# Performance work log

Measured on AMD Instinct MI355X. Metric: run time of the kernel, lower is better.

Reference implementation:

```python
import jax, jax.numpy as jnp
import numpy as np

EPS_BN = 1e-5
EPS_RENORM = 1e-9

def conv_bn_relu(x, W, g, b, m, v):
    # x: [B, Cin, N], W: [Cout, Cin] (1x1 conv, no bias). Eval-mode BN.
    y = jnp.einsum('oi,bin->bon', W, x)
    scale = (g / jnp.sqrt(v + EPS_BN))[None, :, None]
    bias = (b - m * g / jnp.sqrt(v + EPS_BN))[None, :, None]
    return jax.nn.relu(y * scale + bias)

def _make_params(key, cout, cin):
    k1, k2, k3, k4 = jax.random.split(key, 4)
    W = jax.random.normal(k1, (cout, cin), jnp.float32) * (1.0 / np.sqrt(cin))
    g = jax.random.uniform(k2, (cout,), jnp.float32, 0.5, 1.5)
    b = jax.random.normal(k3, (cout,), jnp.float32) * 0.1
    m = jax.random.normal(k4, (cout,), jnp.float32) * 0.1
    v = jax.random.uniform(jax.random.fold_in(key, 7), (cout,), jnp.float32, 0.5, 1.5)
    return W, g, b, m, v

def setup_inputs() -> dict:
    key = jax.random.key(0)
    ks = jax.random.split(key, 6)
    B, C, N = 8, 1024, 2048
    x = jax.random.normal(ks[0], (B, C, N), jnp.float32)
    inp = {'x': x}
    dims = [(1024, 1024), (1024, 1024), (128, 1024), (128, 1024), (1024, 1024)]
    for i, (co, ci) in enumerate(dims):
        W, g, b, m, v = _make_params(ks[i + 1], co, ci)
        inp[f'W{i+1}'] = W
        inp[f'g{i+1}'] = g
        inp[f'b{i+1}'] = b
        inp[f'm{i+1}'] = m
        inp[f'v{i+1}'] = v
    return inp

def reference(x,
              W1, g1, b1, m1, v1,
              W2, g2, b2, m2, v2,
              W3, g3, b3, m3, v3,
              W4, g4, b4, m4, v4,
              W5, g5, b5, m5, v5):
    x1 = conv_bn_relu(x, W1, g1, b1, m1, v1)          # [B,1024,N]
    v_ = conv_bn_relu(x1, W2, g2, b2, m2, v2)         # [B,1024,N]
    q_ = conv_bn_relu(x1, W3, g3, b3, m3, v3)         # [B,128,N]
    k_ = conv_bn_relu(x1, W4, g4, b4, m4, v4)         # [B,128,N]
    # q transposed: [B,N,128] @ [B,128,N] -> [B,N,N]
    scores = jnp.einsum('bcn,bcm->bnm', q_, k_)
    scores = jax.nn.softmax(scores, axis=-1)
    scores = scores / (EPS_RENORM + scores.sum(axis=1, keepdims=True))
    attn = jnp.einsum('bcn,bnm->bcm', v_, scores)     # [B,1024,N]
    x2 = conv_bn_relu(x1 - attn, W5, g5, b5, m5, v5)
    return x1 + x2
```

## Files before the change

kernel.cpp:

```cpp
#include <hip/hip_runtime.h>

typedef unsigned short u16;
using bf16x8 = __attribute__((ext_vector_type(8))) short;
using f32x4  = __attribute__((ext_vector_type(4))) float;

#define CH   1024
#define NP   2048
#define CQ   128

__device__ __forceinline__ float bf2f(u16 u){
  union { unsigned u; float f; } c; c.u = ((unsigned)u) << 16; return c.f;
}
__device__ __forceinline__ u16 f2bf(float f){
  unsigned x = __float_as_uint(f);
  unsigned r = (x + 0x7fffu + ((x >> 16) & 1u)) >> 16;
  return (u16)r;
}

__device__ __forceinline__ void gl2lds16(const u16* g, u16* l){
  __builtin_amdgcn_global_load_lds(
      (const __attribute__((address_space(1))) unsigned int*)(const void*)g,
      (__attribute__((address_space(3))) unsigned int*)(void*)l,
      16, 0, 0);
}

__global__ void ws_marker(float* out, float have_mb){
  out[0] = 1048576.0f + have_mb;
}

__global__ __launch_bounds__(256) void transpose_split(const float* __restrict__ x,
                                                       u16* __restrict__ xh,
                                                       u16* __restrict__ xl){
  const int bb = blockIdx.z;
  const int n0 = blockIdx.x * 64, c0 = blockIdx.y * 64;
  __shared__ float tile[64][65];
  const int t = threadIdx.x;
  const float* xb = x + ((size_t)bb*CH + c0)*NP + n0;
#pragma unroll
  for (int rr = 0; rr < 4; ++rr){
    const int c_l = (t >> 4) + rr*16;
    const int n_l = (t & 15) * 4;
    float4 v = *(const float4*)&xb[(size_t)c_l*NP + n_l];
    tile[c_l][n_l+0] = v.x; tile[c_l][n_l+1] = v.y;
    tile[c_l][n_l+2] = v.z; tile[c_l][n_l+3] = v.w;
  }
  __syncthreads();
  u16* oh = xh + ((size_t)bb*NP + n0)*CH + c0;
  u16* ol = xl + ((size_t)bb*NP + n0)*CH + c0;
#pragma unroll
  for (int rr = 0; rr < 4; ++rr){
    const int n_l = (t >> 4) + rr*16;
    const int c_l = (t & 15) * 4;
    ushort4 h, l;
    float v0 = tile[c_l+0][n_l], v1 = tile[c_l+1][n_l];
    float v2 = tile[c_l+2][n_l], v3 = tile[c_l+3][n_l];
    h.x = f2bf(v0); l.x = f2bf(v0 - bf2f(h.x));
    h.y = f2bf(v1); l.y = f2bf(v1 - bf2f(h.y));
    h.z = f2bf(v2); l.z = f2bf(v2 - bf2f(h.z));
    h.w = f2bf(v3); l.w = f2bf(v3 - bf2f(h.w));
    *(ushort4*)&oh[(size_t)n_l*CH + c_l] = h;
    *(ushort4*)&ol[(size_t)n_l*CH + c_l] = l;
  }
}

__global__ __launch_bounds__(256) void prep_all(
    const float* __restrict__ w0, const float* __restrict__ w1,
    const float* __restrict__ w2, const float* __restrict__ w3,
    const float* __restrict__ w4,
    u16* w1h, u16* w1l, u16* w2h,
    u16* w34h, u16* w34l, u16* w5h,
    const float* g3, const float* b3, const float* m3, const float* v3,
    const float* g4, const float* b4, const float* m4, const float* v4,
    float* p34, float* colsum){
  const int seg = blockIdx.y;
  if (seg == 5){
    for (int i = blockIdx.x*blockDim.x + threadIdx.x; i < 1024; i += gridDim.x*blockDim.x){
      const int grp = i >> 8, j = i & 255;
      const float* pa = (grp==0) ? g3 : (grp==1) ? b3 : (grp==2) ? m3 : v3;
      const float* pb = (grp==0) ? g4 : (grp==1) ? b4 : (grp==2) ? m4 : v4;
      p34[i] = (j < 128) ? pa[j] : pb[j-128];
    }
    return;
  }
  if (seg == 6){
    for (int i = blockIdx.x*blockDim.x + threadIdx.x; i < 8*NP; i += gridDim.x*blockDim.x)
      colsum[i] = 0.f;
    return;
  }
  const float* w; u16 *wh, *wl; int n;
  switch (seg){
    case 0:  w = w0; wh = w1h;           wl = w1l;           n = CH*CH; break;
    case 1:  w = w1; wh = w2h;           wl = nullptr;       n = CH*CH; break;
    case 2:  w = w2; wh = w34h;          wl = w34l;          n = CQ*CH; break;
    case 3:  w = w3; wh = w34h + CQ*CH;  wl = w34l + CQ*CH;  n = CQ*CH; break;
    default: w = w4; wh = w5h;           wl = nullptr;       n = CH*CH; break;
  }
  for (int i = blockIdx.x*blockDim.x + threadIdx.x; i < n; i += gridDim.x*blockDim.x){
    float v = w[i];
    u16 h = f2bf(v);
    wh[i] = h;
    if (wl) wl[i] = f2bf(v - bf2f(h));
  }
}

template<int EPI>
__global__ __launch_bounds__(256, 4) void gemm_plain(
    const u16* __restrict__ A, const u16* __restrict__ B,
    int lda, int ldb, long astr, long bstr, int K,
    void* __restrict__ out0, long ostr, int ldo,
    const float* __restrict__ pg, const float* __restrict__ pb,
    const float* __restrict__ pm, const float* __restrict__ pv,
    const u16* __restrict__ x1h, const u16* __restrict__ x1l,
    const float* __restrict__ cinv, const u16* __restrict__ cbf)
{
  __shared__ __align__(16) u16 sA[8192], sB[8192];
  const int tid  = threadIdx.x;
  const int lane = tid & 63, wave = tid >> 6;
  const int wr = wave & 1, wc = wave >> 1;
  const int l15 = lane & 15, q = lane >> 4;
  const int id = blockIdx.x;
  const int bb = id & 7;
  const int rest = id >> 3;
  const int by = rest & 7;
  const int bx = rest >> 3;
  const u16* Ab = A + (size_t)bb*astr + (size_t)bx*128*lda;
  const u16* Bb = B + (size_t)bb*bstr + (size_t)by*128*ldb;

  f32x4 acc[4][4] = {};
  f32x4 accR[4] = {};

  const int srow = tid >> 3;
  const int schunk = tid & 7;

  for (int kt = 0; kt < K; kt += 64){
#pragma unroll
    for (int r = 0; r < 4; ++r){
      const int row = r*32 + srow;
      const int gc8 = ((schunk ^ (row & 7)) << 3);
      gl2lds16(Ab + (size_t)row*lda + kt + gc8, &sA[r*2048 + tid*8]);
      gl2lds16(Bb + (size_t)row*ldb + kt + gc8, &sB[r*2048 + tid*8]);
    }
    __syncthreads();
#pragma unroll
    for (int s = 0; s < 2; ++s){
      bf16x8 af[4], bfr[4];
#pragma unroll
      for (int i = 0; i < 4; ++i){
        const int ra = wr*64 + i*16 + l15;
        af[i]  = *(const bf16x8*)&sA[ra*64 + (((s*4 + q) ^ (ra & 7)) << 3)];
        const int rb = wc*64 + i*16 + l15;
        bfr[i] = *(const bf16x8*)&sB[rb*64 + (((s*4 + q) ^ (rb & 7)) << 3)];
      }
      if constexpr (EPI == 1){
        const bf16x8 bcs = *(const bf16x8*)&cbf[(size_t)bb*NP + kt + s*32 + q*8];
#pragma unroll
        for (int i = 0; i < 4; ++i)
          accR[i] = __builtin_amdgcn_mfma_f32_16x16x32_bf16(af[i], bcs, accR[i], 0, 0, 0);
      }
#pragma unroll
      for (int i = 0; i < 4; ++i)
#pragma unroll
        for (int j = 0; j < 4; ++j)
          acc[i][j] = __builtin_amdgcn_mfma_f32_16x16x32_bf16(af[i], bfr[j], acc[i][j], 0, 0, 0);
    }
    __syncthreads();
  }

  const int rbase = bx*128 + wr*64;
  const int cbase = by*128 + wc*64;
#pragma unroll
  for (int j = 0; j < 4; ++j){
    const int gc = cbase + j*16 + l15;
    float scale = 0.f, bias = 0.f;
    if (EPI == 0 || EPI == 2){
      scale = pg[gc] * rsqrtf(pv[gc] + 1e-5f);
      bias  = pb[gc] - pm[gc]*scale;
    }
#pragma unroll
    for (int i = 0; i < 4; ++i){
      const int gr0 = rbase + i*16 + q*4;
      if (EPI == 0){
        const float4 cv = *(const float4*)&cinv[(size_t)bb*NP + gr0];
        ushort4 pk;
        pk.x = f2bf(fmaxf(acc[i][j][0]*scale + bias, 0.f) * cv.x);
        pk.y = f2bf(fmaxf(acc[i][j][1]*scale + bias, 0.f) * cv.y);
        pk.z = f2bf(fmaxf(acc[i][j][2]*scale + bias, 0.f) * cv.z);
        pk.w = f2bf(fmaxf(acc[i][j][3]*scale + bias, 0.f) * cv.w);
        *(ushort4*)&((u16*)out0)[(size_t)bb*ostr + (size_t)gc*ldo + gr0] = pk;
      } else if (EPI == 1){
#pragma unroll
        for (int r = 0; r < 4; ++r){
          const int gr = gr0 + r;
          const size_t idx = (size_t)bb*ostr + (size_t)gr*ldo + gc;
          const float rsv = 1.f / (1e-9f + accR[i][r]);
          const float x1v = bf2f(x1h[idx]) + bf2f(x1l[idx]);
          ((u16*)out0)[idx] = f2bf(x1v - acc[i][j][r]*rsv);
        }
      } else {
        float4 o4;
#pragma unroll
        for (int r = 0; r < 4; ++r){
          const int gr = gr0 + r;
          const size_t xidx = (size_t)bb*((size_t)NP*CH) + (size_t)gr*CH + gc;
          const float x2  = fmaxf(acc[i][j][r]*scale + bias, 0.f);
          const float x1v = bf2f(x1h[xidx]) + bf2f(x1l[xidx]);
          (&o4.x)[r] = x1v + x2;
        }
        *(float4*)&((float*)out0)[(size_t)bb*ostr + (size_t)gc*ldo + gr0] = o4;
      }
    }
  }
}

template<int EPI>
__global__ __launch_bounds__(256, 4) void gemm_split3(
    const u16* __restrict__ Ah, const u16* __restrict__ Al,
    const u16* __restrict__ Bh, const u16* __restrict__ Bl,
    int lda, int ldb, long astr, long bstr, int K,
    u16* __restrict__ outH, u16* __restrict__ outL,
    long ostr, int ldo,
    const float* __restrict__ pg, const float* __restrict__ pb,
    const float* __restrict__ pm, const float* __restrict__ pv,
    float* __restrict__ colsum, int gymask, int gyshift)
{
  __shared__ __align__(16) u16 sAh[4096], sAl[4096], sBh[4096], sBl[4096];
  const int tid  = threadIdx.x;
  const int lane = tid & 63, wave = tid >> 6;
  const int wr = wave & 1, wc = wave >> 1;
  const int l15 = lane & 15, q = lane >> 4;
  const int id = blockIdx.x;
  const int bb = id & 7;
  const int rest = id >> 3;
  const int by = rest & gymask;
  const int bx = rest >> gyshift;
  const u16* Abh = Ah + (size_t)bb*astr + (size_t)bx*128*lda;
  const u16* Abl = Al + (size_t)bb*astr + (size_t)bx*128*lda;
  const u16* Bbh = Bh + (size_t)bb*bstr + (size_t)by*128*ldb;
  const u16* Bbl = Bl + (size_t)bb*bstr + (size_t)by*128*ldb;

  f32x4 acc[4][4] = {};

  const int r0 = tid >> 2, r1 = r0 + 64;
  const int cs = (((tid & 3) ^ ((r0 >> 1) & 3)) << 3);

  int offA[4], offB[4];
#pragma unroll
  for (int i = 0; i < 4; ++i){
    const int ra = wr*64 + i*16 + l15;
    offA[i] = ra*32 + ((q ^ ((ra >> 1) & 3)) << 3);
    const int rb = wc*64 + i*16 + l15;
    offB[i] = rb*32 + ((q ^ ((rb >> 1) & 3)) << 3);
  }

  for (int kt = 0; kt < K; kt += 32){
    gl2lds16(Abh + (size_t)r0*lda + kt + cs, &sAh[tid*8]);
    gl2lds16(Abh + (size_t)r1*lda + kt + cs, &sAh[2048 + tid*8]);
    gl2lds16(Abl + (size_t)r0*lda + kt + cs, &sAl[tid*8]);
    gl2lds16(Abl + (size_t)r1*lda + kt + cs, &sAl[2048 + tid*8]);
    gl2lds16(Bbh + (size_t)r0*ldb + kt + cs, &sBh[tid*8]);
    gl2lds16(Bbh + (size_t)r1*ldb + kt + cs, &sBh[2048 + tid*8]);
    gl2lds16(Bbl + (size_t)r0*ldb + kt + cs, &sBl[tid*8]);
    gl2lds16(Bbl + (size_t)r1*ldb + kt + cs, &sBl[2048 + tid*8]);
    __syncthreads();
    bf16x8 ah[4], al[4], bh2[4], bl2[4];
#pragma unroll
    for (int i = 0; i < 4; ++i){
      ah[i] = *(const bf16x8*)&sAh[offA[i]];
      al[i] = *(const bf16x8*)&sAl[offA[i]];
    }
#pragma unroll
    for (int j = 0; j < 4; ++j){
      bh2[j] = *(const bf16x8*)&sBh[offB[j]];
      bl2[j] = *(const bf16x8*)&sBl[offB[j]];
    }
#pragma unroll
    for (int i = 0; i < 4; ++i)
#pragma unroll
      for (int j = 0; j < 4; ++j){
        acc[i][j] = __builtin_amdgcn_mfma_f32_16x16x32_bf16(ah[i], bh2[j], acc[i][j], 0, 0, 0);
        acc[i][j] = __builtin_amdgcn_mfma_f32_16x16x32_bf16(ah[i], bl2[j], acc[i][j], 0, 0, 0);
        acc[i][j] = __builtin_amdgcn_mfma_f32_16x16x32_bf16(al[i], bh2[j], acc[i][j], 0, 0, 0);
      }
    __syncthreads();
  }

  const int rbase = bx*128 + wr*64;
  const int cbase = by*128 + wc*64;

  if constexpr (EPI == 1){
    __shared__ float colpart[128];
    if (tid < 128) colpart[tid] = 0.f;
    __syncthreads();
#pragma unroll
    for (int j = 0; j < 4; ++j){
      const int gc = cbase + j*16 + l15;
      float lsum = 0.f;
#pragma unroll
      for (int i = 0; i < 4; ++i){
        const int gr0 = rbase + i*16 + q*4;
#pragma unroll
        for (int r = 0; r < 4; ++r){
          const float e = __expf(fminf(acc[i][j][r], 85.f));
          outH[(size_t)bb*ostr + (size_t)(gr0 + r)*ldo + gc] = f2bf(e);
          lsum += e;
        }
      }
      atomicAdd(&colpart[wc*64 + j*16 + l15], lsum);
    }
    __syncthreads();
    if (tid < 128) atomicAdd(&colsum[(size_t)bb*NP + (size_t)by*128 + tid], colpart[tid]);
  } else {
#pragma unroll
    for (int j = 0; j < 4; ++j){
      const int gc = cbase + j*16 + l15;
      const float scale = pg[gc] * rsqrtf(pv[gc] + 1e-5f);
      const float bias  = pb[gc] - pm[gc]*scale;
#pragma unroll
      for (int i = 0; i < 4; ++i){
        const int gr0 = rbase + i*16 + q*4;
#pragma unroll
        for (int r = 0; r < 4; ++r){
          const size_t idx = (size_t)bb*ostr + (size_t)(gr0 + r)*ldo + gc;
          const float y = fmaxf(acc[i][j][r]*scale + bias, 0.f);
          const u16 h = f2bf(y);
          outH[idx] = h;
          outL[idx] = f2bf(y - bf2f(h));
        }
      }
    }
  }
}

__global__ __launch_bounds__(256) void colinv_k(const float* __restrict__ cs,
                                                float* __restrict__ ci,
                                                u16* __restrict__ cib, int n){
  const int i = blockIdx.x*blockDim.x + threadIdx.x;
  if (i < n){
    const float v = 1.0f / cs[i];
    ci[i]  = v;
    cib[i] = f2bf(v);
  }
}

extern "C" void kernel_launch(void* const* d_in, const int* in_sizes, int n_in,
                              void* d_out, int out_size, void* d_ws, size_t ws_size,
                              hipStream_t stream){
  const float* x = (const float*)d_in[0];
  const float *W[5], *g[5], *bt[5], *mu[5], *vr[5];
  for (int i = 0; i < 5; ++i){
    W[i]  = (const float*)d_in[1 + 5*i + 0];
    g[i]  = (const float*)d_in[1 + 5*i + 1];
    bt[i] = (const float*)d_in[1 + 5*i + 2];
    mu[i] = (const float*)d_in[1 + 5*i + 3];
    vr[i] = (const float*)d_in[1 + 5*i + 4];
  }

  char* wp = (char*)d_ws;
  size_t off = 0;
  auto take = [&](size_t bytes) -> void* {
    void* p = wp + off;
    off = (off + bytes + 255) & ~(size_t)255;
    return p;
  };
  u16*   xh   = (u16*)take(33554432);
  u16*   xl   = (u16*)take(33554432);
  u16*   x1h  = (u16*)take(33554432);
  u16*   x1l  = (u16*)take(33554432);
  u16*   qkh  = (u16*)take(8388608);
  u16*   qkl  = (u16*)take(8388608);
  float* csum = (float*)take(65536);
  float* cinv = (float*)take(65536);
  u16*   cibf = (u16*)take(32768);
  u16*   w1h  = (u16*)take(2097152);
  u16*   w1l  = (u16*)take(2097152);
  u16*   w2h  = (u16*)take(2097152);
  u16*   w34h = (u16*)take(524288);
  u16*   w34l = (u16*)take(524288);
  u16*   w5h  = (u16*)take(2097152);
  float* p34  = (float*)take(4096);

  if (ws_size < off){
    ws_marker<<<1, 1, 0, stream>>>((float*)d_out, (float)(ws_size >> 20));
    return;
  }

  u16* vh   = xh;
  u16* tt   = xl;
  u16* expS = (u16*)d_out;

  prep_all<<<dim3(256, 7), 256, 0, stream>>>(
      W[0], W[1], W[2], W[3], W[4],
      w1h, w1l, w2h, w34h, w34l, w5h,
      g[2], bt[2], mu[2], vr[2], g[3], bt[3], mu[3], vr[3],
      p34, csum);

  transpose_split<<<dim3(32,16,8), 256, 0, stream>>>(x, xh, xl);

  gemm_split3<0><<<dim3(1024), 256, 0, stream>>>(
      xh, xl, w1h, w1l, CH, CH, (long)NP*CH, 0, CH,
      x1h, x1l, (long)NP*CH, CH, g[0], bt[0], mu[0], vr[0], nullptr, 7, 3);

  gemm_split3<0><<<dim3(256), 256, 0, stream>>>(
      x1h, x1l, w34h, w34l, CH, CH, (long)NP*CH, 0, CH,
      qkh, qkl, (long)NP*256, 256, p34, p34+256, p34+512, p34+768, nullptr, 1, 1);

  gemm_split3<1><<<dim3(2048), 256, 0, stream>>>(
      qkh + 128, qkl + 128, qkh, qkl, 256, 256, (long)NP*256, (long)NP*256, CQ,
      expS, nullptr, (long)NP*NP, NP,
      nullptr, nullptr, nullptr, nullptr, csum, 15, 4);

  colinv_k<<<dim3(64), 256, 0, stream>>>(csum, cinv, cibf, 8*NP);

  gemm_plain<0><<<dim3(1024), 256, 0, stream>>>(
      x1h, w2h, CH, CH, (long)NP*CH, 0, CH,
      vh, (long)CH*NP, NP, g[1], bt[1], mu[1], vr[1],
      nullptr, nullptr, cinv, nullptr);

  gemm_plain<1><<<dim3(1024), 256, 0, stream>>>(
      expS, vh, NP, NP, (long)NP*NP, (long)CH*NP, NP,
      tt, (long)NP*CH, CH, nullptr, nullptr, nullptr, nullptr,
      x1h, x1l, nullptr, cibf);

  gemm_plain<2><<<dim3(1024), 256, 0, stream>>>(
      tt, w5h, CH, CH, (long)NP*CH, 0, CH,
      d_out, (long)CH*NP, NP, g[4], bt[4], mu[4], vr[4],
      x1h, x1l, nullptr, nullptr);
}
```

Measured before the change: 670.1 us.

## Switch GEMMs to 32x32x16 MFMA and compute renorm row sums separately

Both GEMM kernels now issue 32x32x16 bf16 MFMA instructions on 2x2 fragments per wave instead of 16x16x32 on 4x4 fragments, which cuts LDS fragment loads and instruction count. The epilogue index mapping is rewritten to match the 32x32 accumulator layout. The extra rowsum MFMAs that the attention GEMM ran against a bf16 copy of the column inverses are removed. A separate rowsum_dot kernel now computes the renormalisation sums in fp32 and the GEMM reads them, at the cost of one more pass over the 64MB expS matrix.

New measurement: 676.1 us. About the same (+0.9%).

```diff
diff --git a/kernel.cpp b/kernel.cpp
--- a/kernel.cpp
+++ b/kernel.cpp
@@ -2,7 +2,7 @@
 
 typedef unsigned short u16;
 using bf16x8 = __attribute__((ext_vector_type(8))) short;
-using f32x4  = __attribute__((ext_vector_type(4))) float;
+using f32x16 = __attribute__((ext_vector_type(16))) float;
 
 #define CH   1024
 #define NP   2048
@@ -111,13 +111,13 @@
     const float* __restrict__ pg, const float* __restrict__ pb,
     const float* __restrict__ pm, const float* __restrict__ pv,
     const u16* __restrict__ x1h, const u16* __restrict__ x1l,
-    const float* __restrict__ cinv, const u16* __restrict__ cbf)
+    const float* __restrict__ cinv, const float* __restrict__ rsum)
 {
   __shared__ __align__(16) u16 sA[8192], sB[8192];
   const int tid  = threadIdx.x;
   const int lane = tid & 63, wave = tid >> 6;
   const int wr = wave & 1, wc = wave >> 1;
-  const int l15 = lane & 15, q = lane >> 4;
+  const int l31 = lane & 31, h = lane >> 5;
   const int id = blockIdx.x;
   const int bb = id & 7;
   const int rest = id >> 3;
@@ -126,8 +126,7 @@
   const u16* Ab = A + (size_t)bb*astr + (size_t)bx*128*lda;
   const u16* Bb = B + (size_t)bb*bstr + (size_t)by*128*ldb;
 
-  f32x4 acc[4][4] = {};
-  f32x4 accR[4] = {};
+  f32x16 acc[2][2] = {};
 
   const int srow = tid >> 3;
   const int schunk = tid & 7;
@@ -142,26 +141,20 @@
     }
     __syncthreads();
 #pragma unroll
-    for (int s = 0; s < 2; ++s){
-      bf16x8 af[4], bfr[4];
-#pragma unroll
-      for (int i = 0; i < 4; ++i){
-        const int ra = wr*64 + i*16 + l15;
-        af[i]  = *(const bf16x8*)&sA[ra*64 + (((s*4 + q) ^ (ra & 7)) << 3)];
-        const int rb = wc*64 + i*16 + l15;
-        bfr[i] = *(const bf16x8*)&sB[rb*64 + (((s*4 + q) ^ (rb & 7)) << 3)];
+    for (int s = 0; s < 4; ++s){
+      bf16x8 af[2], bfr[2];
+#pragma unroll
+      for (int t = 0; t < 2; ++t){
+        const int ra = wr*64 + t*32 + l31;
+        af[t]  = *(const bf16x8*)&sA[ra*64 + ((((s<<1) + h) ^ (ra & 7)) << 3)];
+        const int rb = wc*64 + t*32 + l31;
+        bfr[t] = *(const bf16x8*)&sB[rb*64 + ((((s<<1) + h) ^ (rb & 7)) << 3)];
       }
-      if constexpr (EPI == 1){
-        const bf16x8 bcs = *(const bf16x8*)&cbf[(size_t)bb*NP + kt + s*32 + q*8];
-#pragma unroll
-        for (int i = 0; i < 4; ++i)
-          accR[i] = __builtin_amdgcn_mfma_f32_16x16x32_bf16(af[i], bcs, accR[i], 0, 0, 0);
-      }
-#pragma unroll
-      for (int i = 0; i < 4; ++i)
-#pragma unroll
-        for (int j = 0; j < 4; ++j)
-          acc[i][j] = __builtin_amdgcn_mfma_f32_16x16x32_bf16(af[i], bfr[j], acc[i][j], 0, 0, 0);
+#pragma unroll
+      for (int i = 0; i < 2; ++i)
+#pragma unroll
+        for (int j = 0; j < 2; ++j)
+          acc[i][j] = __builtin_amdgcn_mfma_f32_32x32x16_bf16(af[i], bfr[j], acc[i][j], 0, 0, 0);
     }
     __syncthreads();
   }
@@ -169,44 +162,47 @@
   const int rbase = bx*128 + wr*64;
   const int cbase = by*128 + wc*64;
 #pragma unroll
-  for (int j = 0; j < 4; ++j){
-    const int gc = cbase + j*16 + l15;
+  for (int j = 0; j < 2; ++j){
+    const int gc = cbase + j*32 + l31;
     float scale = 0.f, bias = 0.f;
     if (EPI == 0 || EPI == 2){
       scale = pg[gc] * rsqrtf(pv[gc] + 1e-5f);
       bias  = pb[gc] - pm[gc]*scale;
     }
 #pragma unroll
-    for (int i = 0; i < 4; ++i){
-      const int gr0 = rbase + i*16 + q*4;
-      if (EPI == 0){
-        const float4 cv = *(const float4*)&cinv[(size_t)bb*NP + gr0];
-        ushort4 pk;
-        pk.x = f2bf(fmaxf(acc[i][j][0]*scale + bias, 0.f) * cv.x);
-        pk.y = f2bf(fmaxf(acc[i][j][1]*scale + bias, 0.f) * cv.y);
-        pk.z = f2bf(fmaxf(acc[i][j][2]*scale + bias, 0.f) * cv.z);
-        pk.w = f2bf(fmaxf(acc[i][j][3]*scale + bias, 0.f) * cv.w);
-        *(ushort4*)&((u16*)out0)[(size_t)bb*ostr + (size_t)gc*ldo + gr0] = pk;
-      } else if (EPI == 1){
-#pragma unroll
-        for (int r = 0; r < 4; ++r){
-          const int gr = gr0 + r;
-          const size_t idx = (size_t)bb*ostr + (size_t)gr*ldo + gc;
-          const float rsv = 1.f / (1e-9f + accR[i][r]);
-          const float x1v = bf2f(x1h[idx]) + bf2f(x1l[idx]);
-          ((u16*)out0)[idx] = f2bf(x1v - acc[i][j][r]*rsv);
+    for (int i = 0; i < 2; ++i){
+#pragma unroll
+      for (int rg = 0; rg < 4; ++rg){
+        const int gr0 = rbase + i*32 + 8*rg + 4*h;
+        if (EPI == 0){
+          const float4 cv = *(const float4*)&cinv[(size_t)bb*NP + gr0];
+          ushort4 pk;
+          pk.x = f2bf(fmaxf(acc[i][j][rg*4+0]*scale + bias, 0.f) * cv.x);
+          pk.y = f2bf(fmaxf(acc[i][j][rg*4+1]*scale + bias, 0.f) * cv.y);
+          pk.z = f2bf(fmaxf(acc[i][j][rg*4+2]*scale + bias, 0.f) * cv.z);
+          pk.w = f2bf(fmaxf(acc[i][j][rg*4+3]*scale + bias, 0.f) * cv.w);
+          *(ushort4*)&((u16*)out0)[(size_t)bb*ostr + (size_t)gc*ldo + gr0] = pk;
+        } else if (EPI == 1){
+          const float4 rv = *(const float4*)&rsum[(size_t)bb*NP + gr0];
+#pragma unroll
+          for (int r = 0; r < 4; ++r){
+            const int gr = gr0 + r;
+            const size_t idx = (size_t)bb*ostr + (size_t)gr*ldo + gc;
+            const float x1v = bf2f(x1h[idx]) + bf2f(x1l[idx]);
+            ((u16*)out0)[idx] = f2bf(x1v - acc[i][j][rg*4+r]*(&rv.x)[r]);
+          }
+        } else {
+          float4 o4;
+#pragma unroll
+          for (int r = 0; r < 4; ++r){
+            const int gr = gr0 + r;
+            const size_t xidx = (size_t)bb*((size_t)NP*CH) + (size_t)gr*CH + gc;
+            const float x2  = fmaxf(acc[i][j][rg*4+r]*scale + bias, 0.f);
+            const float x1v = bf2f(x1h[xidx]) + bf2f(x1l[xidx]);
+            (&o4.x)[r] = x1v + x2;
+          }
+          *(float4*)&((float*)out0)[(size_t)bb*ostr + (size_t)gc*ldo + gr0] = o4;
         }
-      } else {
-        float4 o4;
-#pragma unroll
-        for (int r = 0; r < 4; ++r){
-          const int gr = gr0 + r;
-          const size_t xidx = (size_t)bb*((size_t)NP*CH) + (size_t)gr*CH + gc;
-          const float x2  = fmaxf(acc[i][j][r]*scale + bias, 0.f);
-          const float x1v = bf2f(x1h[xidx]) + bf2f(x1l[xidx]);
-          (&o4.x)[r] = x1v + x2;
-        }
-        *(float4*)&((float*)out0)[(size_t)bb*ostr + (size_t)gc*ldo + gr0] = o4;
       }
     }
   }
@@ -227,7 +223,7 @@
   const int tid  = threadIdx.x;
   const int lane = tid & 63, wave = tid >> 6;
   const int wr = wave & 1, wc = wave >> 1;
-  const int l15 = lane & 15, q = lane >> 4;
+  const int l31 = lane & 31, h = lane >> 5;
   const int id = blockIdx.x;
   const int bb = id & 7;
   const int rest = id >> 3;
@@ -238,19 +234,10 @@
   const u16* Bbh = Bh + (size_t)bb*bstr + (size_t)by*128*ldb;
   const u16* Bbl = Bl + (size_t)bb*bstr + (size_t)by*128*ldb;
 
-  f32x4 acc[4][4] = {};
+  f32x16 acc[2][2] = {};
 
   const int r0 = tid >> 2, r1 = r0 + 64;
   const int cs = (((tid & 3) ^ ((r0 >> 1) & 3)) << 3);
-
-  int offA[4], offB[4];
-#pragma unroll
-  for (int i = 0; i < 4; ++i){
-    const int ra = wr*64 + i*16 + l15;
-    offA[i] = ra*32 + ((q ^ ((ra >> 1) & 3)) << 3);
-    const int rb = wc*64 + i*16 + l15;
-    offB[i] = rb*32 + ((q ^ ((rb >> 1) & 3)) << 3);
-  }
 
   for (int kt = 0; kt < K; kt += 32){
     gl2lds16(Abh + (size_t)r0*lda + kt + cs, &sAh[tid*8]);
@@ -262,25 +249,29 @@
     gl2lds16(Bbl + (size_t)r0*ldb + kt + cs, &sBl[tid*8]);
     gl2lds16(Bbl + (size_t)r1*ldb + kt + cs, &sBl[2048 + tid*8]);
     __syncthreads();
-    bf16x8 ah[4], al[4], bh2[4], bl2[4];
-#pragma unroll
-    for (int i = 0; i < 4; ++i){
-      ah[i] = *(const bf16x8*)&sAh[offA[i]];
-      al[i] = *(const bf16x8*)&sAl[offA[i]];
-    }
-#pragma unroll
-    for (int j = 0; j < 4; ++j){
-      bh2[j] = *(const bf16x8*)&sBh[offB[j]];
-      bl2[j] = *(const bf16x8*)&sBl[offB[j]];
-    }
-#pragma unroll
-    for (int i = 0; i < 4; ++i)
-#pragma unroll
-      for (int j = 0; j < 4; ++j){
-        acc[i][j] = __builtin_amdgcn_mfma_f32_16x16x32_bf16(ah[i], bh2[j], acc[i][j], 0, 0, 0);
-        acc[i][j] = __builtin_amdgcn_mfma_f32_16x16x32_bf16(ah[i], bl2[j], acc[i][j], 0, 0, 0);
-        acc[i][j] = __builtin_amdgcn_mfma_f32_16x16x32_bf16(al[i], bh2[j], acc[i][j], 0, 0, 0);
+#pragma unroll
+    for (int s = 0; s < 2; ++s){
+      bf16x8 ah[2], al[2], bh2[2], bl2[2];
+#pragma unroll
+      for (int t = 0; t < 2; ++t){
+        const int ra = wr*64 + t*32 + l31;
+        const int oa = ra*32 + ((((s<<1) + h) ^ ((ra >> 1) & 3)) << 3);
+        ah[t] = *(const bf16x8*)&sAh[oa];
+        al[t] = *(const bf16x8*)&sAl[oa];
+        const int rb = wc*64 + t*32 + l31;
+        const int ob = rb*32 + ((((s<<1) + h) ^ ((rb >> 1) & 3)) << 3);
+        bh2[t] = *(const bf16x8*)&sBh[ob];
+        bl2[t] = *(const bf16x8*)&sBl[ob];
       }
+#pragma unroll
+      for (int i = 0; i < 2; ++i)
+#pragma unroll
+        for (int j = 0; j < 2; ++j){
+          acc[i][j] = __builtin_amdgcn_mfma_f32_32x32x16_bf16(ah[i], bh2[j], acc[i][j], 0, 0, 0);
+          acc[i][j] = __builtin_amdgcn_mfma_f32_32x32x16_bf16(ah[i], bl2[j], acc[i][j], 0, 0, 0);
+          acc[i][j] = __builtin_amdgcn_mfma_f32_32x32x16_bf16(al[i], bh2[j], acc[i][j], 0, 0, 0);
+        }
+    }
     __syncthreads();
   }
 
@@ -292,39 +283,45 @@
     if (tid < 128) colpart[tid] = 0.f;
     __syncthreads();
 #pragma unroll
-    for (int j = 0; j < 4; ++j){
-      const int gc = cbase + j*16 + l15;
+    for (int j = 0; j < 2; ++j){
+      const int gc = cbase + j*32 + l31;
       float lsum = 0.f;
 #pragma unroll
-      for (int i = 0; i < 4; ++i){
-        const int gr0 = rbase + i*16 + q*4;
-#pragma unroll
-        for (int r = 0; r < 4; ++r){
-          const float e = __expf(fminf(acc[i][j][r], 85.f));
-          outH[(size_t)bb*ostr + (size_t)(gr0 + r)*ldo + gc] = f2bf(e);
-          lsum += e;
+      for (int i = 0; i < 2; ++i){
+#pragma unroll
+        for (int rg = 0; rg < 4; ++rg){
+          const int gr0 = rbase + i*32 + 8*rg + 4*h;
+#pragma unroll
+          for (int r = 0; r < 4; ++r){
+            const float e = __expf(fminf(acc[i][j][rg*4+r], 85.f));
+            outH[(size_t)bb*ostr + (size_t)(gr0 + r)*ldo + gc] = f2bf(e);
+            lsum += e;
+          }
         }
       }
-      atomicAdd(&colpart[wc*64 + j*16 + l15], lsum);
+      atomicAdd(&colpart[wc*64 + j*32 + l31], lsum);
     }
     __syncthreads();
     if (tid < 128) atomicAdd(&colsum[(size_t)bb*NP + (size_t)by*128 + tid], colpart[tid]);
   } else {
 #pragma unroll
-    for (int j = 0; j < 4; ++j){
-      const int gc = cbase + j*16 + l15;
+    for (int j = 0; j < 2; ++j){
+      const int gc = cbase + j*32 + l31;
       const float scale = pg[gc] * rsqrtf(pv[gc] + 1e-5f);
       const float bias  = pb[gc] - pm[gc]*scale;
 #pragma unroll
-      for (int i = 0; i < 4; ++i){
-        const int gr0 = rbase + i*16 + q*4;
-#pragma unroll
-        for (int r = 0; r < 4; ++r){
-          const size_t idx = (size_t)bb*ostr + (size_t)(gr0 + r)*ldo + gc;
-          const float y = fmaxf(acc[i][j][r]*scale + bias, 0.f);
-          const u16 h = f2bf(y);
-          outH[idx] = h;
-          outL[idx] = f2bf(y - bf2f(h));
+      for (int i = 0; i < 2; ++i){
+#pragma unroll
+        for (int rg = 0; rg < 4; ++rg){
+          const int gr0 = rbase + i*32 + 8*rg + 4*h;
+#pragma unroll
+          for (int r = 0; r < 4; ++r){
+            const size_t idx = (size_t)bb*ostr + (size_t)(gr0 + r)*ldo + gc;
+            const float y = fmaxf(acc[i][j][rg*4+r]*scale + bias, 0.f);
+            const u16 hh = f2bf(y);
+            outH[idx] = hh;
+            outL[idx] = f2bf(y - bf2f(hh));
+          }
         }
       }
     }
@@ -332,14 +329,33 @@
 }
 
 __global__ __launch_bounds__(256) void colinv_k(const float* __restrict__ cs,
-                                                float* __restrict__ ci,
-                                                u16* __restrict__ cib, int n){
+                                                float* __restrict__ ci, int n){
   const int i = blockIdx.x*blockDim.x + threadIdx.x;
-  if (i < n){
-    const float v = 1.0f / cs[i];
-    ci[i]  = v;
-    cib[i] = f2bf(v);
-  }
+  if (i < n) ci[i] = 1.0f / cs[i];
+}
+
+__global__ __launch_bounds__(256) void rowsum_dot(const u16* __restrict__ expS,
+                                                  const float* __restrict__ cinv,
+                                                  float* __restrict__ rs){
+  const int row  = blockIdx.x*4 + (threadIdx.x >> 6);
+  const int lane = threadIdx.x & 63;
+  const int b = row >> 11;
+  const u16* e = expS + (size_t)row*NP;
+  const float* ci = cinv + (size_t)b*NP;
+  float s = 0.f;
+#pragma unroll
+  for (int k = 0; k < 4; ++k){
+    const int idx = (k*64 + lane)*8;
+    ushort4 a0 = *(const ushort4*)&e[idx];
+    ushort4 a1 = *(const ushort4*)&e[idx+4];
+    float4 c0 = *(const float4*)&ci[idx];
+    float4 c1 = *(const float4*)&ci[idx+4];
+    s += bf2f(a0.x)*c0.x + bf2f(a0.y)*c0.y + bf2f(a0.z)*c0.z + bf2f(a0.w)*c0.w
+       + bf2f(a1.x)*c1.x + bf2f(a1.y)*c1.y + bf2f(a1.z)*c1.z + bf2f(a1.w)*c1.w;
+  }
+#pragma unroll
+  for (int off2 = 32; off2; off2 >>= 1) s += __shfl_down(s, off2, 64);
+  if (lane == 0) rs[row] = 1.f / (1e-9f + s);
 }
 
 extern "C" void kernel_launch(void* const* d_in, const int* in_sizes, int n_in,
@@ -370,7 +386,7 @@
   u16*   qkl  = (u16*)take(8388608);
   float* csum = (float*)take(65536);
   float* cinv = (float*)take(65536);
-  u16*   cibf = (u16*)take(32768);
+  float* rs   = (float*)take(65536);
   u16*   w1h  = (u16*)take(2097152);
   u16*   w1l  = (u16*)take(2097152);
   u16*   w2h  = (u16*)take(2097152);
@@ -409,7 +425,8 @@
       expS, nullptr, (long)NP*NP, NP,
       nullptr, nullptr, nullptr, nullptr, csum, 15, 4);
 
-  colinv_k<<<dim3(64), 256, 0, stream>>>(csum, cinv, cibf, 8*NP);
+  colinv_k<<<dim3(64), 256, 0, stream>>>(csum, cinv, 8*NP);
+  rowsum_dot<<<dim3(4096), 256, 0, stream>>>(expS, cinv, rs);
 
   gemm_plain<0><<<dim3(1024), 256, 0, stream>>>(
       x1h, w2h, CH, CH, (long)NP*CH, 0, CH,
@@ -419,7 +436,7 @@
   gemm_plain<1><<<dim3(1024), 256, 0, stream>>>(
       expS, vh, NP, NP, (long)NP*NP, (long)CH*NP, NP,
       tt, (long)NP*CH, CH, nullptr, nullptr, nullptr, nullptr,
-      x1h, x1l, nullptr, cibf);
+      x1h, x1l, nullptr, rs);
 
   gemm_plain<2><<<dim3(1024), 256, 0, stream>>>(
       tt, w5h, CH, CH, (long)NP*CH, 0, CH,
```
